# Optimization experiments

Hardware: AMD Instinct MI355X
Metric: run time of the kernel (lower is better)

The kernel has to match this reference:

```python
import jax, jax.numpy as jnp
import numpy as np

B, N, D = 4, 1024, 1024
H, DH = 16, 64
MEM = 16
SCALE = DH ** -0.5
EPS = 1e-6


def setup_inputs() -> dict:
    key = jax.random.key(0)
    ks = jax.random.split(key, 8)
    inner = H * DH
    return {
        "x": jax.random.normal(ks[0], (B, N, D), dtype=jnp.float32),
        "mask": jnp.ones((B, N), dtype=bool),
        "Wq": jax.random.normal(ks[1], (D, inner), dtype=jnp.float32) / np.sqrt(D),
        "Wkv": jax.random.normal(ks[2], (D, 2 * inner), dtype=jnp.float32) / np.sqrt(D),
        "Wo": jax.random.normal(ks[3], (inner, D), dtype=jnp.float32) / np.sqrt(inner),
        "mem_k": jax.random.normal(ks[4], (H, MEM, DH), dtype=jnp.float32),
        "mem_v": jax.random.normal(ks[5], (H, MEM, DH), dtype=jnp.float32),
        "th_pre": jax.random.normal(ks[6], (H, H), dtype=jnp.float32) / np.sqrt(H),
        "th_post": jax.random.normal(ks[7], (H, H), dtype=jnp.float32) / np.sqrt(H),
    }


def _l2norm(t):
    return t * jax.lax.rsqrt(jnp.sum(t * t, axis=-1, keepdims=True) + EPS)


def reference(x, mask, Wq, Wkv, Wo, mem_k, mem_v, th_pre, th_post):
    b, n, _ = x.shape
    # projections: b n (h d) -> b h n d
    q = (x @ Wq).reshape(b, n, H, DH).transpose(0, 2, 1, 3)
    kv = (x @ Wkv).reshape(b, n, 2, H, DH)
    k = kv[:, :, 0].transpose(0, 2, 1, 3)
    v = kv[:, :, 1].transpose(0, 2, 1, 3)
    # qk-norm (l2 normalize along head dim)
    q = _l2norm(q)
    k = _l2norm(k)
    # memory key/values: prepend MEM learned slots
    k = jnp.concatenate([jnp.broadcast_to(mem_k[None], (b, H, MEM, DH)), k], axis=2)
    v = jnp.concatenate([jnp.broadcast_to(mem_v[None], (b, H, MEM, DH)), v], axis=2)
    jk = n + MEM
    dots = jnp.einsum('bhid,bhjd->bhij', q, k) * SCALE
    # talking heads pre-softmax: mix across head dim
    dots = jnp.einsum('bhij,hg->bgij', dots, th_pre)
    # causal mask (mem slots always visible) + key padding mask
    i_pos = jnp.arange(n)[:, None]
    j_pos = jnp.arange(jk)[None, :] - MEM
    causal_ok = j_pos <= i_pos  # [n, jk]
    key_mask = jnp.concatenate([jnp.ones((b, MEM), dtype=bool), mask], axis=1)  # [b, jk]
    full_mask = causal_ok[None, None] & key_mask[:, None, None, :]
    neg = jnp.finfo(dots.dtype).min
    dots = jnp.where(full_mask, dots, neg)
    attn = jax.nn.softmax(dots, axis=-1)
    # talking heads post-softmax
    attn = jnp.einsum('bhij,hg->bgij', attn, th_post)
    out = jnp.einsum('bhij,bhjd->bhid', attn, v)
    out = out.transpose(0, 2, 1, 3).reshape(b, n, H * DH)
    return out @ Wo, attn
```

## Files before the change

kernel.cpp:

```cpp
#include <hip/hip_runtime.h>

#define B_ 4
#define N_ 1024
#define D_ 1024
#define H_ 16
#define DH_ 64
#define MEM_ 16
#define JK_ 1040
#define JKP_ 1056
#define SCALE_ 0.125f
#define EPS_ 1e-6f
#define BHN_ 65536
#define SP_ 1092

typedef short bf16x8 __attribute__((ext_vector_type(8)));
typedef float f32x4 __attribute__((ext_vector_type(4)));
typedef _Float16 f16x4 __attribute__((ext_vector_type(4)));
typedef _Float16 f16x8 __attribute__((ext_vector_type(8)));
typedef ushort u16x8 __attribute__((ext_vector_type(8)));

union F16x8u { f16x4 h[2]; f16x8 v; };

__device__ __forceinline__ ushort f2b(float f) {
    unsigned u = __builtin_bit_cast(unsigned, f);
    unsigned r = (u + 0x7fffu + ((u >> 16) & 1u)) >> 16;
    return (ushort)r;
}

__device__ __forceinline__ void gload16(const ushort* g, ushort* l) {
    __builtin_amdgcn_global_load_lds((__attribute__((address_space(1))) void*)g,
                                     (__attribute__((address_space(3))) void*)l, 16, 0, 0);
}

__device__ __forceinline__ void snake(int blk, int& b, int& pair, int& strip) {
    int q = blk >> 8, c = blk & 255;
    b = c & 3;
    int r = c >> 2;
    pair = r & 31;
    strip = ((r >> 5) << 1) | q;
}

__global__ void k_cast_x(const float* __restrict__ x, ushort* __restrict__ xb, int n4) {
    int i = blockIdx.x * blockDim.x + threadIdx.x;
    if (i >= n4) return;
    float4 v = ((const float4*)x)[i];
    ushort4 o;
    o.x = f2b(v.x); o.y = f2b(v.y); o.z = f2b(v.z); o.w = f2b(v.w);
    ((ushort4*)xb)[i] = o;
}

__global__ void k_tcast(const float* __restrict__ src, ushort* __restrict__ dst, int R, int C) {
    __shared__ float t[32][33];
    int bx = blockIdx.x * 32, by = blockIdx.y * 32;
    int x = bx + threadIdx.x;
    for (int k = 0; k < 32; k += 8) {
        int y = by + threadIdx.y + k;
        t[threadIdx.y + k][threadIdx.x] = src[(size_t)y * C + x];
    }
    __syncthreads();
    int xo = by + threadIdx.x;
    for (int k = 0; k < 32; k += 8) {
        int yo = bx + threadIdx.y + k;
        dst[(size_t)yo * R + xo] = f2b(t[threadIdx.x][threadIdx.y + k]);
    }
}

__global__ __launch_bounds__(256) void k_gemm(const ushort* __restrict__ A, const ushort* __restrict__ BT,
                                              float* __restrict__ C, int ldc) {
    __shared__ ushort lA[4096];
    __shared__ ushort lB[4096];
    int tid = threadIdx.x, w = tid >> 6, lane = tid & 63;
    int l16 = lane & 15, quad = lane >> 4;
    int wr = w >> 1, wc = w & 1;
    int m0 = blockIdx.y * 128, n0 = blockIdx.x * 128;
    f32x4 acc[4][4];
#pragma unroll
    for (int mi = 0; mi < 4; mi++)
#pragma unroll
        for (int ni = 0; ni < 4; ni++) acc[mi][ni] = (f32x4){0.f, 0.f, 0.f, 0.f};

    int srow = (lane >> 2);
    int cg = lane & 3;
    for (int k0 = 0; k0 < 1024; k0 += 32) {
#pragma unroll
        for (int i = 0; i < 2; i++) {
            int row = w * 32 + i * 16 + srow;
            int cgS = cg ^ ((row >> 1) & 3);
            gload16(A + (size_t)(m0 + row) * 1024 + k0 + cgS * 8, lA + w * 1024 + i * 512);
            gload16(BT + (size_t)(n0 + row) * 1024 + k0 + cgS * 8, lB + w * 1024 + i * 512);
        }
        __syncthreads();
        bf16x8 af[4], bfr[4];
#pragma unroll
        for (int mi = 0; mi < 4; mi++) {
            int arow = wr * 64 + mi * 16 + l16;
            af[mi] = *(const bf16x8*)(lA + arow * 32 + (quad ^ ((arow >> 1) & 3)) * 8);
        }
#pragma unroll
        for (int ni = 0; ni < 4; ni++) {
            int brow = wc * 64 + ni * 16 + l16;
            bfr[ni] = *(const bf16x8*)(lB + brow * 32 + (quad ^ ((brow >> 1) & 3)) * 8);
        }
#pragma unroll
        for (int mi = 0; mi < 4; mi++)
#pragma unroll
            for (int ni = 0; ni < 4; ni++)
                acc[mi][ni] = __builtin_amdgcn_mfma_f32_16x16x32_bf16(af[mi], bfr[ni], acc[mi][ni], 0, 0, 0);
        __syncthreads();
    }
#pragma unroll
    for (int mi = 0; mi < 4; mi++)
#pragma unroll
        for (int ni = 0; ni < 4; ni++)
#pragma unroll
            for (int r = 0; r < 4; r++)
                C[(size_t)(m0 + wr * 64 + mi * 16 + quad * 4 + r) * ldc + n0 + wc * 64 + ni * 16 + l16] =
                    acc[mi][ni][r];
}

__global__ __launch_bounds__(256) void k_norm_qk(const float* __restrict__ proj,
                                                 ushort* __restrict__ qw, ushort* __restrict__ kw) {
    int w = threadIdx.x >> 6, lane = threadIdx.x & 63;
    int id = blockIdx.x * 4 + w;
    int qk = id & 1;
    int h = (id >> 1) & 15;
    int i = (id >> 5) & 1023;
    int b = id >> 15;
    float v = proj[(size_t)(b * N_ + i) * 3072 + qk * 1024 + h * 64 + lane];
    float ss = v * v;
#pragma unroll
    for (int m = 1; m < 64; m <<= 1) ss += __shfl_xor(ss, m);
    float r = rsqrtf(ss + EPS_);
    ushort o = f2b(v * r);
    if (qk == 0)
        qw[((size_t)(b * H_ + h) * N_ + i) * DH_ + lane] = o;
    else
        kw[((size_t)(b * H_ + h) * JKP_ + MEM_ + i) * DH_ + lane] = o;
}

__global__ __launch_bounds__(256) void k_v_transpose(const float* __restrict__ proj, _Float16* __restrict__ vt) {
    __shared__ float t[64][65];
    int bh = blockIdx.x, c = blockIdx.y;
    int b = bh >> 4, h = bh & 15;
    int i0 = c * 64;
#pragma unroll
    for (int l = 0; l < 16; l++) {
        int idx = threadIdx.x + l * 256;
        int il = idx >> 6, d = idx & 63;
        t[il][d] = proj[(size_t)(b * N_ + i0 + il) * 3072 + 2048 + h * 64 + d];
    }
    __syncthreads();
#pragma unroll
    for (int l = 0; l < 16; l++) {
        int idx = threadIdx.x + l * 256;
        int dr = idx >> 6, ic = idx & 63;
        vt[((size_t)(b * H_ + h) * DH_ + dr) * JKP_ + MEM_ + i0 + ic] = (_Float16)t[ic][dr];
    }
}

__global__ void k_mem_fill(const float* __restrict__ mk, const float* __restrict__ mv,
                           ushort* __restrict__ kw, _Float16* __restrict__ vt) {
    int b = blockIdx.x >> 4, h = blockIdx.x & 15;
#pragma unroll
    for (int l = 0; l < 4; l++) {
        int idx = threadIdx.x + l * 256;
        int j = idx >> 6, d = idx & 63;
        kw[((size_t)(b * H_ + h) * JKP_ + j) * DH_ + d] = f2b(mk[(h * MEM_ + j) * DH_ + d]);
        vt[((size_t)(b * H_ + h) * DH_ + d) * JKP_ + j] = (_Float16)mv[(h * MEM_ + j) * DH_ + d];
        kw[((size_t)(b * H_ + h) * JKP_ + JK_ + j) * DH_ + d] = 0;
        vt[((size_t)(b * H_ + h) * DH_ + d) * JKP_ + JK_ + j] = (_Float16)0.f;
    }
}

__global__ void k_zerofill(float* __restrict__ attn) {
    int blk = blockIdx.x;
    int ti = blk & 63, g = (blk >> 6) & 15, b = blk >> 10;
    int zs = 32 * (((ti + 1) >> 1) + 1);
    if (zs >= JK_) return;
    int cols4 = (JK_ - zs) >> 2;
    f32x4 z = (f32x4){0.f, 0.f, 0.f, 0.f};
    for (int r = 0; r < 16; r++) {
        f32x4* base = (f32x4*)(attn + ((size_t)(b * H_ + g) * N_ + ti * 16 + r) * JK_ + zs);
        for (int c4 = threadIdx.x; c4 < cols4; c4 += 256) __builtin_nontemporal_store(z, base + c4);
    }
}


__device__ __forceinline__ void qk_tile(_Float16* ldsD, const ushort* kp,
                                        bf16x8 qa0, bf16x8 qa1, int j0, int h, int l16, int quad) {
#pragma unroll
    for (int js = 0; js < 4; js++) {
        f32x4 d = (f32x4){0.f, 0.f, 0.f, 0.f};
        const ushort* kpp = kp + (size_t)(j0 + js * 16 + l16) * DH_ + quad * 8;
        d = __builtin_amdgcn_mfma_f32_16x16x32_bf16(qa0, *(const bf16x8*)kpp, d, 0, 0, 0);
        d = __builtin_amdgcn_mfma_f32_16x16x32_bf16(qa1, *(const bf16x8*)(kpp + 32), d, 0, 0, 0);
#pragma unroll
        for (int r = 0; r < 4; r++)
            ldsD[h * SP_ + (quad * 4 + r) * 68 + js * 16 + l16] = (_Float16)(d[r] * SCALE_);
    }
}

__device__ __forceinline__ f32x4 premix_frag(const _Float16* ldsD, f16x4 thA,
                                             int row, int jg, int l16, int quad) {
    f16x4 bf;
#pragma unroll
    for (int t = 0; t < 4; t++) bf[t] = ldsD[(quad * 4 + t) * SP_ + row * 68 + jg * 16 + l16];
    return __builtin_amdgcn_mfma_f32_16x16x16f16(thA, bf, (f32x4){0.f, 0.f, 0.f, 0.f}, 0, 0, 0);
}

__global__ __launch_bounds__(512, 4) void k_attn_pass1(
    const ushort* __restrict__ qw, const ushort* __restrict__ kw,
    const float* __restrict__ thpre, float* __restrict__ Sws) {
    __shared__ _Float16 ldsD[16 * SP_];
    int tid = threadIdx.x;
    int w = tid >> 6, lane = tid & 63, l16 = lane & 15, quad = lane >> 4;
    int b, pair, strip;
    snake(blockIdx.x, b, pair, strip);

    f16x4 thA;
#pragma unroll
    for (int t = 0; t < 4; t++) thA[t] = (_Float16)thpre[(quad * 4 + t) * 16 + l16];

    for (int half = 0; half < 2; half++) {
        int ti = half ? (63 - pair) : pair;
        int i0 = ti * 16;
        int Ut = (ti + 1) >> 2;
        int u0 = (strip + ti) & 3;

        bf16x8 qa[2][2];
#pragma unroll
        for (int hi = 0; hi < 2; hi++) {
            int h = w + hi * 8;
            const ushort* qp = qw + ((size_t)(b * H_ + h) * N_ + i0 + l16) * DH_ + quad * 8;
            qa[hi][0] = *(const bf16x8*)(qp);
            qa[hi][1] = *(const bf16x8*)(qp + 32);
        }
        float Ssum[2][4];
#pragma unroll
        for (int rr = 0; rr < 2; rr++)
#pragma unroll
            for (int r = 0; r < 4; r++) Ssum[rr][r] = 0.f;

        for (int u = u0; u <= Ut; u += 4) {
            int j0 = u * 64;
#pragma unroll
            for (int hi = 0; hi < 2; hi++) {
                int h = w + hi * 8;
                qk_tile(ldsD, kw + (size_t)(b * H_ + h) * JKP_ * DH_, qa[hi][0], qa[hi][1], j0, h, l16, quad);
            }
            __syncthreads();
#pragma unroll
            for (int rr = 0; rr < 2; rr++) {
                int row = w + rr * 8;
#pragma unroll
                for (int jg = 0; jg < 4; jg++) {
                    f32x4 L = premix_frag(ldsD, thA, row, jg, l16, quad);
                    int j = j0 + jg * 16 + l16;
                    bool valid = (j - MEM_) <= (i0 + row);
#pragma unroll
                    for (int r = 0; r < 4; r++) Ssum[rr][r] += valid ? __expf(L[r]) : 0.f;
                }
            }
            __syncthreads();
        }
#pragma unroll
        for (int rr = 0; rr < 2; rr++)
#pragma unroll
            for (int r = 0; r < 4; r++) {
                float s = Ssum[rr][r];
                s += __shfl_xor(s, 1);
                s += __shfl_xor(s, 2);
                s += __shfl_xor(s, 4);
                s += __shfl_xor(s, 8);
                Ssum[rr][r] = s;
            }
        if (l16 == 0) {
#pragma unroll
            for (int rr = 0; rr < 2; rr++)
#pragma unroll
                for (int r = 0; r < 4; r++)
                    Sws[(size_t)strip * BHN_ + (size_t)(b * H_ + quad * 4 + r) * N_ + i0 + w + rr * 8] =
                        Ssum[rr][r];
        }
    }
}

__global__ __launch_bounds__(512, 4) void k_attnmix(
    const ushort* __restrict__ qw, const ushort* __restrict__ kw,
    const float* __restrict__ Sws, const float* __restrict__ thpre,
    const float* __restrict__ thpost, const _Float16* __restrict__ vt,
    float* __restrict__ attn, _Float16* __restrict__ outp) {
    __shared__ _Float16 ldsDP[16 * SP_];
    __shared__ float inv[16][16];
    int tid = threadIdx.x;
    int w = tid >> 6, lane = tid & 63, l16 = lane & 15, quad = lane >> 4;
    int b, pair, strip;
    snake(blockIdx.x, b, pair, strip);

    f16x4 thA, thP;
#pragma unroll
    for (int t = 0; t < 4; t++) {
        thA[t] = (_Float16)thpre[(quad * 4 + t) * 16 + l16];
        thP[t] = (_Float16)thpost[(quad * 4 + t) * 16 + l16];
    }

    for (int half = 0; half < 2; half++) {
        int ti = half ? (63 - pair) : pair;
        int i0 = ti * 16;
        int Ut = (ti + 1) >> 2;
        int u0 = (strip + ti) & 3;

        __syncthreads();
        if (tid < 256) {
            int g = tid >> 4, r = tid & 15;
            size_t base = (size_t)(b * H_ + g) * N_ + i0 + r;
            inv[g][r] = 1.f / (Sws[base] + Sws[(size_t)BHN_ + base] +
                               Sws[2 * (size_t)BHN_ + base] + Sws[3 * (size_t)BHN_ + base]);
        }
        __syncthreads();
        float invr[2][4];
#pragma unroll
        for (int rr = 0; rr < 2; rr++)
#pragma unroll
            for (int r = 0; r < 4; r++) invr[rr][r] = inv[quad * 4 + r][w + rr * 8];

        bf16x8 qa[2][2];
#pragma unroll
        for (int hi = 0; hi < 2; hi++) {
            int h = w + hi * 8;
            const ushort* qp = qw + ((size_t)(b * H_ + h) * N_ + i0 + l16) * DH_ + quad * 8;
            qa[hi][0] = *(const bf16x8*)(qp);
            qa[hi][1] = *(const bf16x8*)(qp + 32);
        }
        f32x4 macc[2][4];
#pragma unroll
        for (int hi = 0; hi < 2; hi++)
#pragma unroll
            for (int dt = 0; dt < 4; dt++) macc[hi][dt] = (f32x4){0.f, 0.f, 0.f, 0.f};

        for (int u = u0; u <= Ut; u += 4) {
            int j0 = u * 64;
#pragma unroll
            for (int hi = 0; hi < 2; hi++) {
                int h = w + hi * 8;
                qk_tile(ldsDP, kw + (size_t)(b * H_ + h) * JKP_ * DH_, qa[hi][0], qa[hi][1], j0, h, l16, quad);
            }
            __syncthreads();
#pragma unroll
            for (int rr = 0; rr < 2; rr++) {
                int row = w + rr * 8;
#pragma unroll
                for (int jg = 0; jg < 4; jg++) {
                    f32x4 L = premix_frag(ldsDP, thA, row, jg, l16, quad);
                    int j = j0 + jg * 16 + l16;
                    bool valid = (j - MEM_) <= (i0 + row);
                    bool jok = j < JK_;
                    f16x4 pf;
#pragma unroll
                    for (int r = 0; r < 4; r++) {
                        float p = valid ? __expf(L[r]) * invr[rr][r] : 0.f;
                        pf[r] = (_Float16)p;
                    }
                    f32x4 am = __builtin_amdgcn_mfma_f32_16x16x16f16(thP, pf, (f32x4){0.f, 0.f, 0.f, 0.f}, 0, 0, 0);
#pragma unroll
                    for (int r = 0; r < 4; r++) {
                        if (jok)
                            __builtin_nontemporal_store(
                                am[r], &attn[((size_t)(b * H_ + quad * 4 + r) * N_ + i0 + row) * JK_ + j]);
                        ldsDP[(quad * 4 + r) * SP_ + row * 68 + jg * 16 + l16] = (_Float16)am[r];
                    }
                }
            }
            __syncthreads();
#pragma unroll
            for (int hi = 0; hi < 2; hi++) {
                int h = w + hi * 8;
                const _Float16* pb = ldsDP + h * SP_ + l16 * 68 + quad * 8;
                F16x8u pa0, pa1;
                pa0.h[0] = *(const f16x4*)(pb);
                pa0.h[1] = *(const f16x4*)(pb + 4);
                pa1.h[0] = *(const f16x4*)(pb + 32);
                pa1.h[1] = *(const f16x4*)(pb + 36);
                const _Float16* vp = vt + ((size_t)(b * H_ + h) * DH_ + l16) * JKP_ + j0 + quad * 8;
#pragma unroll
                for (int dt = 0; dt < 4; dt++) {
                    macc[hi][dt] = __builtin_amdgcn_mfma_f32_16x16x32_f16(
                        pa0.v, *(const f16x8*)(vp + (size_t)dt * 16 * JKP_), macc[hi][dt], 0, 0, 0);
                    macc[hi][dt] = __builtin_amdgcn_mfma_f32_16x16x32_f16(
                        pa1.v, *(const f16x8*)(vp + (size_t)dt * 16 * JKP_ + 32), macc[hi][dt], 0, 0, 0);
                }
            }
        }
        _Float16* op = outp + (size_t)strip * ((size_t)B_ * H_ * N_ * DH_);
#pragma unroll
        for (int hi = 0; hi < 2; hi++) {
            int h = w + hi * 8;
#pragma unroll
            for (int dt = 0; dt < 4; dt++)
#pragma unroll
                for (int r = 0; r < 4; r++)
                    op[((size_t)(b * H_ + h) * N_ + i0 + quad * 4 + r) * DH_ + dt * 16 + l16] =
                        (_Float16)macc[hi][dt][r];
        }
    }
}

__global__ void k_outcombine(const _Float16* __restrict__ op, ushort* __restrict__ xo) {
    int i8 = blockIdx.x * 256 + threadIdx.x;
    int d8 = i8 & 7, g = (i8 >> 3) & 15, i = (i8 >> 7) & 1023, b = i8 >> 17;
    size_t src8 = ((size_t)(b * H_ + g) * N_ + i) * 8 + d8;
    const size_t STR8 = (size_t)BHN_ * 8;
    f16x8 s0 = ((const f16x8*)op)[src8];
    f16x8 s1 = ((const f16x8*)op)[src8 + STR8];
    f16x8 s2 = ((const f16x8*)op)[src8 + 2 * STR8];
    f16x8 s3 = ((const f16x8*)op)[src8 + 3 * STR8];
    u16x8 o;
#pragma unroll
    for (int k = 0; k < 8; k++) o[k] = f2b((float)s0[k] + (float)s1[k] + (float)s2[k] + (float)s3[k]);
    ((u16x8*)xo)[i8] = o;
}

extern "C" void kernel_launch(void* const* d_in, const int* in_sizes, int n_in,
                              void* d_out, int out_size, void* d_ws, size_t ws_size,
                              hipStream_t stream) {
    const float* x = (const float*)d_in[0];
    const float* Wq = (const float*)d_in[2];
    const float* Wkv = (const float*)d_in[3];
    const float* Wo = (const float*)d_in[4];
    const float* mk = (const float*)d_in[5];
    const float* mv = (const float*)d_in[6];
    const float* thpre = (const float*)d_in[7];
    const float* thpost = (const float*)d_in[8];

    float* out = (float*)d_out;
    float* attn = out + (size_t)B_ * N_ * D_;

    char* ws = (char*)d_ws;
    ushort* WoT = (ushort*)(ws + 0);
    _Float16* vt = (_Float16*)(ws + 2097152);
    ushort* xb = (ushort*)(ws + 10747904);
    float* Sws = (float*)(ws + 10752000);
    ushort* WT = (ushort*)(ws + 19136512);
    ushort* qw = (ushort*)(ws + 25427968);
    ushort* kw = (ushort*)(ws + 33816576);
    float* proj = (float*)(ws + 42467328);
    _Float16* outp = (_Float16*)(ws + 42467328);
    ushort* xo = (ushort*)(ws + 76021760);
    if (ws_size < 92798976) return;

    k_cast_x<<<4096, 256, 0, stream>>>(x, xb, (B_ * N_ * D_) / 4);
    dim3 tb(32, 8);
    k_tcast<<<dim3(32, 32), tb, 0, stream>>>(Wq, WT, 1024, 1024);
    k_tcast<<<dim3(64, 32), tb, 0, stream>>>(Wkv, WT + 1024 * 1024, 1024, 2048);
    k_tcast<<<dim3(32, 32), tb, 0, stream>>>(Wo, WoT, 1024, 1024);
    k_gemm<<<dim3(24, 32), 256, 0, stream>>>(xb, WT, proj, 3072);
    k_norm_qk<<<32768, 256, 0, stream>>>(proj, qw, kw);
    k_v_transpose<<<dim3(64, 16), 256, 0, stream>>>(proj, vt);
    k_mem_fill<<<64, 256, 0, stream>>>(mk, mv, kw, vt);
    k_zerofill<<<4096, 256, 0, stream>>>(attn);
    k_attn_pass1<<<512, 512, 0, stream>>>(qw, kw, thpre, Sws);
    k_attnmix<<<512, 512, 0, stream>>>(qw, kw, Sws, thpre, thpost, vt, attn, outp);
    k_outcombine<<<2048, 256, 0, stream>>>(outp, xo);
    k_gemm<<<dim3(8, 32), 256, 0, stream>>>(xo, WoT, out, 1024);
}
```

Baseline: 559.2 us.

## Fuse attn zero-fill into pass1, use exp2 with log2e-scaled premix, raise occupancy

Removes the separate zero-fill kernel and instead has pass1 blocks write zeros to the masked upper-triangle attn tiles in the loop iterations beyond the causal limit, folding that store traffic into a kernel that is otherwise compute bound. The pre-softmax talking-heads matrix is pre-multiplied by log2(e) so softmax can use exp2f instead of __expf. Launch bounds for both attention kernels are raised from 4 to 6 waves per SIMD, which pressures register allocation and risks spills. Zero stores now depend on the per-strip loop coverage matching the old zero region.

```diff
diff --git a/kernel.cpp b/kernel.cpp
--- a/kernel.cpp
+++ b/kernel.cpp
@@ -12,6 +12,7 @@
 #define EPS_ 1e-6f
 #define BHN_ 65536
 #define SP_ 1092
+#define LOG2E_ 1.4426950408889634f
 
 typedef short bf16x8 __attribute__((ext_vector_type(8)));
 typedef float f32x4 __attribute__((ext_vector_type(4)));
@@ -172,19 +173,6 @@
     }
 }
 
-__global__ void k_zerofill(float* __restrict__ attn) {
-    int blk = blockIdx.x;
-    int ti = blk & 63, g = (blk >> 6) & 15, b = blk >> 10;
-    int zs = 32 * (((ti + 1) >> 1) + 1);
-    if (zs >= JK_) return;
-    int cols4 = (JK_ - zs) >> 2;
-    f32x4 z = (f32x4){0.f, 0.f, 0.f, 0.f};
-    for (int r = 0; r < 16; r++) {
-        f32x4* base = (f32x4*)(attn + ((size_t)(b * H_ + g) * N_ + ti * 16 + r) * JK_ + zs);
-        for (int c4 = threadIdx.x; c4 < cols4; c4 += 256) __builtin_nontemporal_store(z, base + c4);
-    }
-}
-
 
 __device__ __forceinline__ void qk_tile(_Float16* ldsD, const ushort* kp,
                                         bf16x8 qa0, bf16x8 qa1, int j0, int h, int l16, int quad) {
@@ -208,9 +196,9 @@
     return __builtin_amdgcn_mfma_f32_16x16x16f16(thA, bf, (f32x4){0.f, 0.f, 0.f, 0.f}, 0, 0, 0);
 }
 
-__global__ __launch_bounds__(512, 4) void k_attn_pass1(
+__global__ __launch_bounds__(512, 6) void k_attn_pass1(
     const ushort* __restrict__ qw, const ushort* __restrict__ kw,
-    const float* __restrict__ thpre, float* __restrict__ Sws) {
+    const float* __restrict__ thpre, float* __restrict__ Sws, float* __restrict__ attn) {
     __shared__ _Float16 ldsD[16 * SP_];
     int tid = threadIdx.x;
     int w = tid >> 6, lane = tid & 63, l16 = lane & 15, quad = lane >> 4;
@@ -219,7 +207,9 @@
 
     f16x4 thA;
 #pragma unroll
-    for (int t = 0; t < 4; t++) thA[t] = (_Float16)thpre[(quad * 4 + t) * 16 + l16];
+    for (int t = 0; t < 4; t++) thA[t] = (_Float16)(thpre[(quad * 4 + t) * 16 + l16] * LOG2E_);
+
+    int zg = tid >> 5, zrr = tid & 31, zrow = zrr >> 1, zch = zrr & 1;
 
     for (int half = 0; half < 2; half++) {
         int ti = half ? (63 - pair) : pair;
@@ -241,27 +231,36 @@
 #pragma unroll
             for (int r = 0; r < 4; r++) Ssum[rr][r] = 0.f;
 
-        for (int u = u0; u <= Ut; u += 4) {
+        for (int u = u0; u <= 16; u += 4) {
             int j0 = u * 64;
-#pragma unroll
-            for (int hi = 0; hi < 2; hi++) {
-                int h = w + hi * 8;
-                qk_tile(ldsD, kw + (size_t)(b * H_ + h) * JKP_ * DH_, qa[hi][0], qa[hi][1], j0, h, l16, quad);
+            if (u <= Ut) {
+#pragma unroll
+                for (int hi = 0; hi < 2; hi++) {
+                    int h = w + hi * 8;
+                    qk_tile(ldsD, kw + (size_t)(b * H_ + h) * JKP_ * DH_, qa[hi][0], qa[hi][1], j0, h, l16, quad);
+                }
+                __syncthreads();
+#pragma unroll
+                for (int rr = 0; rr < 2; rr++) {
+                    int row = w + rr * 8;
+#pragma unroll
+                    for (int jg = 0; jg < 4; jg++) {
+                        f32x4 L = premix_frag(ldsD, thA, row, jg, l16, quad);
+                        int j = j0 + jg * 16 + l16;
+                        bool valid = (j - MEM_) <= (i0 + row);
+#pragma unroll
+                        for (int r = 0; r < 4; r++) Ssum[rr][r] += valid ? exp2f(L[r]) : 0.f;
+                    }
+                }
+                __syncthreads();
+            } else {
+                int jend = JK_ - j0;
+                float* base = attn + ((size_t)(b * H_ + zg) * N_ + i0 + zrow) * JK_ + j0 + zch * 32;
+                f32x4 z = (f32x4){0.f, 0.f, 0.f, 0.f};
+#pragma unroll
+                for (int k = 0; k < 8; k++)
+                    if (zch * 32 + k * 4 < jend) __builtin_nontemporal_store(z, (f32x4*)(base + k * 4));
             }
-            __syncthreads();
-#pragma unroll
-            for (int rr = 0; rr < 2; rr++) {
-                int row = w + rr * 8;
-#pragma unroll
-                for (int jg = 0; jg < 4; jg++) {
-                    f32x4 L = premix_frag(ldsD, thA, row, jg, l16, quad);
-                    int j = j0 + jg * 16 + l16;
-                    bool valid = (j - MEM_) <= (i0 + row);
-#pragma unroll
-                    for (int r = 0; r < 4; r++) Ssum[rr][r] += valid ? __expf(L[r]) : 0.f;
-                }
-            }
-            __syncthreads();
         }
 #pragma unroll
         for (int rr = 0; rr < 2; rr++)
@@ -285,7 +284,7 @@
     }
 }
 
-__global__ __launch_bounds__(512, 4) void k_attnmix(
+__global__ __launch_bounds__(512, 6) void k_attnmix(
     const ushort* __restrict__ qw, const ushort* __restrict__ kw,
     const float* __restrict__ Sws, const float* __restrict__ thpre,
     const float* __restrict__ thpost, const _Float16* __restrict__ vt,
@@ -300,7 +299,7 @@
     f16x4 thA, thP;
 #pragma unroll
     for (int t = 0; t < 4; t++) {
-        thA[t] = (_Float16)thpre[(quad * 4 + t) * 16 + l16];
+        thA[t] = (_Float16)(thpre[(quad * 4 + t) * 16 + l16] * LOG2E_);
         thP[t] = (_Float16)thpost[(quad * 4 + t) * 16 + l16];
     }
 
@@ -358,7 +357,7 @@
                     f16x4 pf;
 #pragma unroll
                     for (int r = 0; r < 4; r++) {
-                        float p = valid ? __expf(L[r]) * invr[rr][r] : 0.f;
+                        float p = valid ? exp2f(L[r]) * invr[rr][r] : 0.f;
                         pf[r] = (_Float16)p;
                     }
                     f32x4 am = __builtin_amdgcn_mfma_f32_16x16x16f16(thP, pf, (f32x4){0.f, 0.f, 0.f, 0.f}, 0, 0, 0);
@@ -457,8 +456,7 @@
     k_norm_qk<<<32768, 256, 0, stream>>>(proj, qw, kw);
     k_v_transpose<<<dim3(64, 16), 256, 0, stream>>>(proj, vt);
     k_mem_fill<<<64, 256, 0, stream>>>(mk, mv, kw, vt);
-    k_zerofill<<<4096, 256, 0, stream>>>(attn);
-    k_attn_pass1<<<512, 512, 0, stream>>>(qw, kw, thpre, Sws);
+    k_attn_pass1<<<512, 512, 0, stream>>>(qw, kw, thpre, Sws, attn);
     k_attnmix<<<512, 512, 0, stream>>>(qw, kw, Sws, thpre, thpost, vt, attn, outp);
     k_outcombine<<<2048, 256, 0, stream>>>(outp, xo);
     k_gemm<<<dim3(8, 32), 256, 0, stream>>>(xo, WoT, out, 1024);
```

Result: slower. 924.3 us (+65.3%).
